# Optimization experiments

Measured on AMD Instinct MI355X. Metric: run time of the kernel, lower is better.

## Reference

```python
import jax, jax.numpy as jnp
import numpy as np

# Faithful JAX port of DNCWrapper wrapping ixaxaar/pytorch-dnc DNC:
# input_dim=output_dim=512, 2 DNC layers, 2-layer LSTM controller each,
# nr_cells=16, cell_size=20, read_heads=4, clip=20, independent_linears, batch_first.
B, T, IN, H = 128, 32, 512, 512
M, Wc, R = 16, 20, 4
RW = R * Wc                        # 80 = read-vector width
NN_IN = IN + RW                    # 592 controller input (== H + RW since IN == H)
IFACE = RW + R + Wc + 1 + Wc + Wc + R + 1 + 1 + 3 * R  # 163 interface width
L = 2                              # DNC layers
CLIP = 20.0
EPS = 1e-6                         # cosine-similarity delta
DELTA = 5e-6                       # usage floor before cumprod


def setup_inputs():
    key = jax.random.key(0)
    ks = jax.random.split(key, 13)
    p = lambda k, shape: jax.random.normal(k, shape, jnp.float32) * 0.05
    return {
        "x": jax.random.normal(ks[0], (B, T, IN), jnp.float32),
        "W_ih0": p(ks[1], (L, 4 * H, NN_IN)),
        "W_hh0": p(ks[2], (L, 4 * H, H)),
        "b_ih0": p(ks[3], (L, 4 * H)),
        "b_hh0": p(ks[4], (L, 4 * H)),
        "W_ih1": p(ks[5], (L, 4 * H, H)),
        "W_hh1": p(ks[6], (L, 4 * H, H)),
        "b_ih1": p(ks[7], (L, 4 * H)),
        "b_hh1": p(ks[8], (L, 4 * H)),
        "W_iface": p(ks[9], (L, IFACE, H)),
        "b_iface": p(ks[10], (L, IFACE)),
        "W_out": p(ks[11], (IN, H + RW)),
        "b_out": p(ks[12], (IN,)),
    }


def _lstm_cell(inp, h, c, Wih, Whh, bih, bhh):
    g = inp @ Wih.T + bih + h @ Whh.T + bhh
    i, f, gg, o = jnp.split(g, 4, axis=1)  # pytorch gate order i,f,g,o
    c = jax.nn.sigmoid(f) * c + jax.nn.sigmoid(i) * jnp.tanh(gg)
    h = jax.nn.sigmoid(o) * jnp.tanh(c)
    return h, c


def _content(mem, keys, strengths):
    # cosine-similarity content addressing, softmax over memory cells
    mn = mem / (jnp.linalg.norm(mem, axis=2, keepdims=True) + EPS)
    kn = keys / (jnp.linalg.norm(keys, axis=2, keepdims=True) + EPS)
    cos = jnp.einsum('brw,bmw->brm', kn, mn)
    return jax.nn.softmax(cos * strengths[:, :, None], axis=2)


def _memory_step(xi, mst, Wi, bi):
    memory, link, prec, rw, ww, usage = mst
    iface = xi @ Wi.T + bi
    idx = [0]
    def take(n):
        v = iface[:, idx[0]:idx[0] + n]; idx[0] += n; return v
    read_keys = jnp.tanh(take(RW)).reshape(-1, R, Wc)
    read_str = jax.nn.softplus(take(R))
    write_key = jnp.tanh(take(Wc))
    write_str = jax.nn.softplus(take(1))
    erase = jax.nn.sigmoid(take(Wc))
    write_vec = jnp.tanh(take(Wc))
    free_g = jax.nn.sigmoid(take(R))
    alloc_g = jax.nn.sigmoid(take(1))
    write_g = jax.nn.sigmoid(take(1))
    read_modes = jax.nn.softmax(take(3 * R).reshape(-1, R, 3), axis=2)
    # usage update (single write head: 1 - prod(1-ww) == ww)
    usage = usage + (1.0 - usage) * ww
    psi = jnp.prod(1.0 - free_g[:, :, None] * rw, axis=1)
    usage = usage * psi
    # content lookup with write key on pre-write memory
    wcw = _content(memory, write_key[:, None, :], write_str)[:, 0]  # (b,M)
    # allocation: ascending usage sort + exclusive cumprod, then unsort
    u = DELTA + (1.0 - DELTA) * usage
    phi = jnp.argsort(u, axis=1)
    su = jnp.take_along_axis(u, phi, axis=1)
    ones = jnp.ones((u.shape[0], 1), u.dtype)
    prod_ex = jnp.cumprod(jnp.concatenate([ones, su], axis=1), axis=1)[:, :-1]
    sa = (1.0 - su) * prod_ex
    alloc = jnp.take_along_axis(sa, jnp.argsort(phi, axis=1), axis=1)
    # write weighting
    ww = write_g * (alloc_g * alloc + (1.0 - alloc_g) * wcw)
    # erase + write
    memory = memory * (1.0 - ww[:, :, None] * erase[:, None, :]) \
             + ww[:, :, None] * write_vec[:, None, :]
    # temporal link matrix + precedence
    prev_scale = 1.0 - ww[:, :, None] - ww[:, None, :]
    link = (prev_scale * link + ww[:, :, None] * prec[:, None, :]) \
           * (1.0 - jnp.eye(M, dtype=link.dtype))
    prec = (1.0 - jnp.sum(ww, axis=1, keepdims=True)) * prec + ww
    # read: content + forward/backward link traversal, mixed by read modes
    rcw = _content(memory, read_keys, read_str)  # (b,R,M)
    fwd = jnp.einsum('bij,brj->bri', link, rw)
    bwd = jnp.einsum('bri,bij->brj', rw, link)
    rw = read_modes[:, :, 0:1] * bwd + read_modes[:, :, 1:2] * fwd + read_modes[:, :, 2:3] * rcw
    read_vecs = jnp.einsum('brm,bmw->brw', rw, memory).reshape(-1, RW)
    return read_vecs, (memory, link, prec, rw, ww, usage)


def _forward(x, W_ih0, W_hh0, b_ih0, b_hh0, W_ih1, W_hh1, b_ih1, b_hh1,
             W_iface, b_iface, W_out, b_out):
    b = x.shape[0]
    z = lambda *s: jnp.zeros(s, x.dtype)
    carry0 = (z(L, 2, b, H), z(L, 2, b, H), z(L, b, M, Wc), z(L, b, M, M),
              z(L, b, M), z(L, b, R, M), z(L, b, M), z(L, b, M))
    # repo precomputes inputs[t] = cat(x_t, initial last_read) for ALL t (last_read is
    # NOT threaded across time, only memory/LSTM state is) -- reproduced faithfully
    last_read = z(b, RW)

    def step(carry, x_t):
        h, c, mem, link, prec, rw, ww, usage = carry
        inp = jnp.concatenate([x_t, last_read], axis=1)
        new = [[] for _ in range(8)]
        for l in range(L):
            h0, c0 = _lstm_cell(inp, h[l, 0], c[l, 0], W_ih0[l], W_hh0[l], b_ih0[l], b_hh0[l])
            h1, c1 = _lstm_cell(h0, h[l, 1], c[l, 1], W_ih1[l], W_hh1[l], b_ih1[l], b_hh1[l])
            out = jnp.clip(h1, -CLIP, CLIP)
            read_vecs, mst = _memory_step(out, (mem[l], link[l], prec[l], rw[l], ww[l], usage[l]),
                                          W_iface[l], b_iface[l])
            inp = jnp.concatenate([out, read_vecs], axis=1)  # feeds next DNC layer
            new[0].append(jnp.stack([h0, h1])); new[1].append(jnp.stack([c0, c1]))
            for i, a in enumerate(mst):
                new[2 + i].append(a)
        y_t = inp @ W_out.T + b_out  # final output layer: nn_output_size -> input_size
        return tuple(jnp.stack(n) for n in new), y_t

    _, ys = jax.lax.scan(step, carry0, jnp.moveaxis(x, 1, 0))
    return jnp.moveaxis(ys, 0, 1)  # (B, T, IN), batch_first


def reference(x, W_ih0, W_hh0, b_ih0, b_hh0, W_ih1, W_hh1, b_ih1, b_hh1,
              W_iface, b_iface, W_out, b_out):
    return _forward(x, W_ih0, W_hh0, b_ih0, b_hh0, W_ih1, W_hh1, b_ih1, b_hh1,
                    W_iface, b_iface, W_out, b_out)
```

## Files before the change

kernel.cpp:

```cpp
#include <hip/hip_runtime.h>
#include <hip/hip_bf16.h>
#include <math.h>

#define B_ 128
#define T_ 32
#define IN_ 512
#define H_ 512
#define M_ 16
#define WC_ 20
#define R_ 4
#define RW_ 80
#define NNIN_ 592
#define IFACE_ 163
#define IFP_ 176
#define K1P_ 1120
#define K2P_ 1024
#define KOP_ 608
#define CLIP_ 20.0f
#define EPS_ 1e-6f
#define DELTA_ 5e-6f

typedef __bf16 bf16x8 __attribute__((ext_vector_type(8)));
typedef float f32x4 __attribute__((ext_vector_type(4)));

__device__ __forceinline__ float sigmoidf_(float x) { return 1.0f / (1.0f + __expf(-x)); }
__device__ __forceinline__ float tanhf_(float x) {
    float e = __expf(-2.f * fabsf(x));
    float t = (1.f - e) / (1.f + e);
    return copysignf(t, x);
}
__device__ __forceinline__ float softplusf_(float x) {
    return fmaxf(x, 0.0f) + log1pf(__expf(-fabsf(x)));
}
__device__ __forceinline__ void split2(float v, __bf16* hp, __bf16* lp) {
    __bf16 h = (__bf16)v;
    *hp = h;
    *lp = (__bf16)(v - (float)h);
}
#define WBAR_() __builtin_amdgcn_wave_barrier()

struct P {
    const float *x, *bih0, *bhh0, *bih1, *bhh1, *bif0, *bif1, *bout;
    float* out;
    __bf16 *a10[4];
    __bf16 *a11[4];
    __bf16 *a20[4];
    __bf16 *a21[4];
    __bf16 *y[4];
    float *c00, *c01, *c10, *c11;
    float *mem0, *link0, *prec0, *rw0, *ww0, *us0;
    float *mem1, *link1, *prec1, *rw1, *ww1, *us1;
    __bf16 *w10, *w20, *w11, *w21, *wo;
    __bf16 *wif0h, *wif0l, *wif1h, *wif1l;
    float *S0[2], *S1[2];
};

__device__ __forceinline__ void gemm_lstm_tile2(
    int tid, int jt, int mt0, float* red,
    const __bf16* A, int KS,
    const __bf16* W, int nsteps,
    const float* b1, const float* b2, float* cst,
    __bf16* d1, int st1, int off1,
    __bf16* d2, int st2, int off2, int clip2)
{
    const int wave = tid >> 6, lane = tid & 63;
    const int l15 = lane & 15, quad = lane >> 4;
    const int j0 = jt * 16, m0 = mt0 * 16;

    f32x4 acc0[4], acc1[4];
    #pragma unroll
    for (int g = 0; g < 4; ++g)
        #pragma unroll
        for (int i = 0; i < 4; ++i) { acc0[g][i] = 0.f; acc1[g][i] = 0.f; }

    const int ks = (wave * nsteps) >> 2;
    const int ke = ((wave + 1) * nsteps) >> 2;

    size_t aoff0 = (size_t)(m0 + l15) * KS + ks * 32 + quad * 8;
    size_t aoff1 = aoff0 + (size_t)16 * KS;
    size_t woff[4];
    #pragma unroll
    for (int g = 0; g < 4; ++g)
        woff[g] = (size_t)(g * 512 + j0 + l15) * KS + ks * 32 + quad * 8;

    for (int s = ks; s < ke; ++s) {
        bf16x8 ah0 = *(const bf16x8*)(A + aoff0);
        bf16x8 ah1 = *(const bf16x8*)(A + aoff1);
        aoff0 += 32; aoff1 += 32;
        #pragma unroll
        for (int g = 0; g < 4; ++g) {
            bf16x8 wh = *(const bf16x8*)(W + woff[g]);
            woff[g] += 32;
            acc0[g] = __builtin_amdgcn_mfma_f32_16x16x32_bf16(ah0, wh, acc0[g], 0, 0, 0);
            acc1[g] = __builtin_amdgcn_mfma_f32_16x16x32_bf16(ah1, wh, acc1[g], 0, 0, 0);
        }
    }

    const int col = j0 + l15;
    float bg[4];
    #pragma unroll
    for (int g = 0; g < 4; ++g) bg[g] = b1[g * 512 + col] + b2[g * 512 + col];

    #pragma unroll
    for (int pair = 0; pair < 2; ++pair) {
        #pragma unroll
        for (int g = 0; g < 4; ++g)
            #pragma unroll
            for (int r = 0; r < 4; ++r)
                red[(g * 4 + r) * 256 + wave * 64 + lane] =
                    pair ? acc1[g][r] : acc0[g][r];
        __syncthreads();

        const int m = m0 + pair * 16 + quad * 4 + wave;
        float gv[4];
        #pragma unroll
        for (int g = 0; g < 4; ++g) {
            const float* rg = red + (g * 4 + wave) * 256;
            gv[g] = rg[lane] + rg[64 + lane] + rg[128 + lane] + rg[192 + lane] + bg[g];
        }
        float cold = cst[m * H_ + col];
        float cn = sigmoidf_(gv[1]) * cold + sigmoidf_(gv[0]) * tanhf_(gv[2]);
        cst[m * H_ + col] = cn;
        float h = sigmoidf_(gv[3]) * tanhf_(cn);
        d1[(size_t)m * st1 + off1 + col] = (__bf16)h;
        float h2 = clip2 ? fminf(fmaxf(h, -CLIP_), CLIP_) : h;
        d2[(size_t)m * st2 + off2 + col] = (__bf16)h2;
        if (pair == 0) __syncthreads();
    }
}

__device__ __forceinline__ void gemm_plain_tile(
    int tid, int nt, int mt, float* red,
    const __bf16* A, int AS,
    const __bf16* W, int WS,
    int nsteps, const float* bias, float* C, int ldc)
{
    const int wave = tid >> 6, lane = tid & 63;
    const int l15 = lane & 15, quad = lane >> 4;
    const int n0 = nt * 16, m0 = mt * 16;

    f32x4 acc;
    #pragma unroll
    for (int i = 0; i < 4; ++i) acc[i] = 0.f;

    const int ks = (wave * nsteps) >> 2;
    const int ke = ((wave + 1) * nsteps) >> 2;

    size_t aoff = (size_t)(m0 + l15) * AS + ks * 32 + quad * 8;
    size_t woff = (size_t)(n0 + l15) * WS + ks * 32 + quad * 8;

    for (int s = ks; s < ke; ++s) {
        bf16x8 ah = *(const bf16x8*)(A + aoff);
        bf16x8 wh = *(const bf16x8*)(W + woff);
        aoff += 32; woff += 32;
        acc = __builtin_amdgcn_mfma_f32_16x16x32_bf16(ah, wh, acc, 0, 0, 0);
    }

    #pragma unroll
    for (int r = 0; r < 4; ++r) red[r * 256 + wave * 64 + lane] = acc[r];
    __syncthreads();

    const int col = n0 + l15;
    const int m = m0 + quad * 4 + wave;
    const float* rg = red + wave * 256;
    float v = rg[lane] + rg[64 + lane] + rg[128 + lane] + rg[192 + lane] + bias[col];
    C[(size_t)m * ldc + col] = v;
}

__device__ __forceinline__ void gemm_iface_tile(
    int tid, int jt, int mt, float* red,
    const __bf16* A, int AS,
    const __bf16* Wh, const __bf16* Wl,
    const float* bif, float* Sout)
{
    const int wave = tid >> 6, lane = tid & 63;
    const int l15 = lane & 15, quad = lane >> 4;
    const int n0 = jt * 16, m0 = mt * 16;

    f32x4 acc;
    #pragma unroll
    for (int i = 0; i < 4; ++i) acc[i] = 0.f;

    size_t aoff = (size_t)(m0 + l15) * AS + wave * 128 + quad * 8;
    size_t woff = (size_t)(n0 + l15) * 512 + wave * 128 + quad * 8;

    #pragma unroll
    for (int s = 0; s < 4; ++s) {
        bf16x8 ah = *(const bf16x8*)(A + aoff);
        bf16x8 wh = *(const bf16x8*)(Wh + woff);
        bf16x8 wl = *(const bf16x8*)(Wl + woff);
        aoff += 32; woff += 32;
        acc = __builtin_amdgcn_mfma_f32_16x16x32_bf16(ah, wh, acc, 0, 0, 0);
        acc = __builtin_amdgcn_mfma_f32_16x16x32_bf16(ah, wl, acc, 0, 0, 0);
    }

    #pragma unroll
    for (int r = 0; r < 4; ++r) red[r * 256 + wave * 64 + lane] = acc[r];
    __syncthreads();

    const int o = n0 + l15;
    if (o < IFACE_) {
        const int m = m0 + quad * 4 + wave;
        const float* rg = red + wave * 256;
        float v = rg[lane] + rg[64 + lane] + rg[128 + lane] + rg[192 + lane] + bif[o];
        float rr;
        if (o < 80)        rr = tanhf_(v);
        else if (o < 84)   rr = softplusf_(v);
        else if (o < 104)  rr = tanhf_(v);
        else if (o < 105)  rr = softplusf_(v);
        else if (o < 125)  rr = sigmoidf_(v);
        else if (o < 145)  rr = tanhf_(v);
        else if (o < 151)  rr = sigmoidf_(v);
        else               rr = v;
        Sout[(size_t)m * IFP_ + o] = rr;
    }
}

__device__ void mem_batch(int b, int wl, float* W, const float* Sbuf,
    float* mem, float* link, float* prec, float* rw,
    float* ww, float* usage, __bf16* rv, int rvst)
{
    for (int i = wl; i < IFACE_; i += 64) W[i] = Sbuf[(size_t)b * IFP_ + i];
    if (wl < M_) W[224 + wl] = prec[(size_t)b * M_ + wl];
    W[240 + wl] = rw[(size_t)b * R_ * M_ + wl];
    #pragma unroll
    for (int k = 0; k < 4; ++k)
        W[368 + wl + 64 * k] = link[(size_t)b * M_ * M_ + wl + 64 * k];
    #pragma unroll
    for (int k = 0; k < 5; ++k)
        W[624 + wl + 64 * k] = mem[(size_t)b * M_ * WC_ + wl + 64 * k];
    WBAR_();

    if (wl < R_) {
        float a0 = W[151 + wl * 3], a1 = W[152 + wl * 3], a2 = W[153 + wl * 3];
        float mx = fmaxf(a0, fmaxf(a1, a2));
        float e0 = __expf(a0 - mx), e1 = __expf(a1 - mx), e2 = __expf(a2 - mx);
        float s = e0 + e1 + e2;
        W[164 + wl * 3] = e0 / s; W[165 + wl * 3] = e1 / s; W[166 + wl * 3] = e2 / s;
    }
    WBAR_();

    if (wl < M_) {
        const int m = wl;
        float wwold = ww[(size_t)b * M_ + m];
        float u = usage[(size_t)b * M_ + m];
        u = u + (1.f - u) * wwold;
        float psi = 1.f;
        #pragma unroll
        for (int r = 0; r < R_; ++r) psi *= (1.f - W[145 + r] * W[240 + r * 16 + m]);
        u *= psi;

        float kn2 = 0.f, mn2 = 0.f, dot = 0.f;
        #pragma unroll
        for (int w = 0; w < WC_; ++w) {
            float kv = W[84 + w], mv = W[624 + m * WC_ + w];
            kn2 += kv * kv; mn2 += mv * mv; dot += kv * mv;
        }
        float c = dot / ((sqrtf(kn2) + EPS_) * (sqrtf(mn2) + EPS_)) * W[104];
        float mx = c;
        #pragma unroll
        for (int off = 8; off; off >>= 1) mx = fmaxf(mx, __shfl_xor(mx, off, 16));
        float e = __expf(c - mx);
        float se = e;
        #pragma unroll
        for (int off = 8; off; off >>= 1) se += __shfl_xor(se, off, 16);
        float wcw = e / se;

        float uu = DELTA_ + (1.f - DELTA_) * u;
        int rank = 0;
        #pragma unroll
        for (int j = 0; j < 16; ++j) {
            float uj = __shfl(uu, j, 16);
            if (uj < uu || (uj == uu && j < m)) ++rank;
        }
        float prod = 1.f;
        #pragma unroll
        for (int j = 0; j < 16; ++j) {
            float uj = __shfl(uu, j, 16);
            int   rj = __shfl(rank, j, 16);
            if (rj < rank) prod *= uj;
        }
        float alloc = (1.f - uu) * prod;

        float ag = W[149], wg = W[150];
        float wwn = wg * (ag * alloc + (1.f - ag) * wcw);
        float sw = wwn;
        #pragma unroll
        for (int off = 8; off; off >>= 1) sw += __shfl_xor(sw, off, 16);

        W[208 + m] = wwn;
        usage[(size_t)b * M_ + m] = u;
        ww[(size_t)b * M_ + m]    = wwn;
        prec[(size_t)b * M_ + m]  = (1.f - sw) * W[224 + m] + wwn;
    }
    WBAR_();

    #pragma unroll
    for (int k = 0; k < 5; ++k) {
        int i = wl + 64 * k;
        int m = i / WC_, w = i - m * WC_;
        float nm = W[624 + i] * (1.f - W[208 + m] * W[105 + w]) + W[208 + m] * W[125 + w];
        W[624 + i] = nm;
        mem[(size_t)b * M_ * WC_ + i] = nm;
    }
    #pragma unroll
    for (int k = 0; k < 4; ++k) {
        int i = wl + 64 * k;
        int ii = i >> 4, jj = i & 15;
        float v = (1.f - W[208 + ii] - W[208 + jj]) * W[368 + i] + W[208 + ii] * W[224 + jj];
        if (ii == jj) v = 0.f;
        W[368 + i] = v;
        link[(size_t)b * M_ * M_ + i] = v;
    }
    WBAR_();

    {
        const int r = wl >> 4, m = wl & 15;
        float kn2 = 0.f, mn2 = 0.f, dot = 0.f;
        #pragma unroll
        for (int w = 0; w < WC_; ++w) {
            float kv = W[r * WC_ + w], mv = W[624 + m * WC_ + w];
            kn2 += kv * kv; mn2 += mv * mv; dot += kv * mv;
        }
        float c = dot / ((sqrtf(kn2) + EPS_) * (sqrtf(mn2) + EPS_)) * W[80 + r];
        float mx = c;
        #pragma unroll
        for (int off = 8; off; off >>= 1) mx = fmaxf(mx, __shfl_xor(mx, off, 16));
        float e = __expf(c - mx);
        float se = e;
        #pragma unroll
        for (int off = 8; off; off >>= 1) se += __shfl_xor(se, off, 16);
        float rc = e / se;

        float fwd = 0.f, bwd = 0.f;
        #pragma unroll
        for (int j = 0; j < M_; ++j) fwd += W[368 + m * 16 + j] * W[240 + r * 16 + j];
        #pragma unroll
        for (int i2 = 0; i2 < M_; ++i2) bwd += W[240 + r * 16 + i2] * W[368 + i2 * 16 + m];
        float v = W[164 + r * 3 + 0] * bwd + W[164 + r * 3 + 1] * fwd + W[164 + r * 3 + 2] * rc;
        W[304 + wl] = v;
        rw[(size_t)b * R_ * M_ + wl] = v;
    }
    WBAR_();

    #pragma unroll
    for (int k = 0; k < 2; ++k) {
        int i = wl + 64 * k;
        if (i < RW_) {
            int r = i / WC_, w = i - r * WC_;
            float s = 0.f;
            #pragma unroll
            for (int m = 0; m < M_; ++m) s += W[304 + r * 16 + m] * W[624 + m * WC_ + w];
            rv[(size_t)b * rvst + IN_ + i] = (__bf16)s;
        }
    }
}

__device__ void mem_group4(int bbase, int tid, float* smem, const float* Sbuf,
    float* mem, float* link, float* prec, float* rw, float* ww, float* usage,
    __bf16* rv, int rvst)
{
    const int wave = tid >> 6, wl = tid & 63;
    mem_batch(bbase + wave, wl, smem + wave * 1024, Sbuf,
              mem, link, prec, rw, ww, usage, rv, rvst);
}

__global__ __launch_bounds__(256, 6) void slot_kernel(P p, int s)
{
    __shared__ float smem[4096];
    const int blk = blockIdx.x, tid = threadIdx.x;
    const int xcd = blk & 7, k = blk >> 3;

    if (k < 4) {
        int t = s - 3;
        if (t >= 0 && t < T_) {
            int i = xcd * 4 + k;
            mem_group4(i * 4, tid, smem, p.S0[t & 1],
                p.mem0, p.link0, p.prec0, p.rw0, p.ww0, p.us0,
                p.a11[t & 3], K1P_);
        }
    } else if (k < 8) {
        int t = s - 7;
        if (t >= 0 && t < T_) {
            int i = xcd * 4 + (k - 4);
            mem_group4(i * 4, tid, smem, p.S1[t & 1],
                p.mem1, p.link1, p.prec1, p.rw1, p.ww1, p.us1,
                p.y[t & 3], KOP_);
        }
    } else if (k < 24) {
        int t = s;
        if (t < T_) {
            int j = k - 8;
            gemm_lstm_tile2(tid, xcd * 4 + (j & 3), (j >> 2) * 2, smem,
                p.a10[t & 3], K2P_, p.w10, K2P_ / 32,
                p.bih0, p.bhh0, p.c00,
                p.a10[(t + 1) & 3], K2P_, 512,
                p.a20[t & 3], K2P_, 0, 0);
        }
    } else if (k < 40) {
        int t = s - 1;
        if (t >= 0 && t < T_) {
            int j = k - 24;
            gemm_lstm_tile2(tid, xcd * 4 + (j & 3), (j >> 2) * 2, smem,
                p.a20[t & 3], K2P_, p.w20, K2P_ / 32,
                p.bih1, p.bhh1, p.c01,
                p.a20[(t + 1) & 3], K2P_, H_,
                p.a11[t & 3], K1P_, 0, 1);
        }
    } else if (k < 56) {
        int t = s - 4;
        if (t >= 0 && t < T_) {
            int j = k - 40;
            gemm_lstm_tile2(tid, xcd * 4 + (j & 3), (j >> 2) * 2, smem,
                p.a11[t & 3], K1P_, p.w11, K1P_ / 32,
                p.bih0 + 2048, p.bhh0 + 2048, p.c10,
                p.a11[(t + 1) & 3], K1P_, NNIN_,
                p.a21[t & 3], K2P_, 0, 0);
        }
    } else if (k < 72) {
        int t = s - 5;
        if (t >= 0 && t < T_) {
            int j = k - 56;
            gemm_lstm_tile2(tid, xcd * 4 + (j & 3), (j >> 2) * 2, smem,
                p.a21[t & 3], K2P_, p.w21, K2P_ / 32,
                p.bih1 + 2048, p.bhh1 + 2048, p.c11,
                p.a21[(t + 1) & 3], K2P_, H_,
                p.y[t & 3], KOP_, 0, 1);
        }
    } else if (k < 104) {
        int t = s - 8;
        if (t >= 0 && t < T_) {
            int j = k - 72;
            gemm_plain_tile(tid, xcd * 4 + (j & 3), j >> 2, smem,
                p.y[t & 3], KOP_, p.wo, KOP_, KOP_ / 32,
                p.bout, p.out + (size_t)t * IN_, T_ * IN_);
        }
    } else if (k < 115) {
        int t = s - 2;
        if (t >= 0 && t < T_) {
            int j = k - 104;
            gemm_iface_tile(tid, j, xcd, smem,
                p.a11[t & 3], K1P_,
                p.wif0h, p.wif0l, p.bif0, p.S0[t & 1]);
        }
    } else if (k < 126) {
        int t = s - 6;
        if (t >= 0 && t < T_) {
            int j = k - 115;
            gemm_iface_tile(tid, j, xcd, smem,
                p.y[t & 3], KOP_,
                p.wif1h, p.wif1l, p.bif1, p.S1[t & 1]);
        }
    } else {
        int tn = s + 1;
        if (tn < T_) {
            int c = xcd * 4 + (k - 126);
            for (int i = c * 256 + tid; i < B_ * IN_; i += 32 * 256) {
                int b = i >> 9, j = i & 511;
                float v = p.x[((size_t)b * T_ + tn) * IN_ + j];
                p.a10[tn & 3][(size_t)b * K2P_ + j] = (__bf16)v;
            }
        }
    }
}

struct ConvArgs { const float* s1; const float* s2; __bf16* dst; int s1s, K1, K2, Kd; };
struct ConvArgs4 { ConvArgs a[4]; };

__global__ __launch_bounds__(256) void conv_lstm(ConvArgs4 ca)
{
    ConvArgs c = ca.a[blockIdx.z];
    int k = blockIdx.x * 256 + threadIdx.x;
    if (k >= c.Kd) return;
    int n = blockIdx.y;
    float v = 0.f;
    if (k < c.K1) v = c.s1[(size_t)n * c.s1s + k];
    else if (k < c.K1 + c.K2) v = c.s2[(size_t)n * c.K2 + (k - c.K1)];
    c.dst[(size_t)n * c.Kd + k] = (__bf16)v;
}

__global__ __launch_bounds__(256) void conv_hi(
    const float* __restrict__ s1, int K1, const float* __restrict__ s2, int K2,
    int Nsrc, __bf16* __restrict__ hi, int Kd)
{
    int k = blockIdx.x * 256 + threadIdx.x;
    int n = blockIdx.y;
    if (k >= Kd) return;
    float v = 0.f;
    if (n < Nsrc) {
        if (k < K1) v = s1[(size_t)n * K1 + k];
        else if (k < K1 + K2) v = s2[(size_t)n * K2 + (k - K1)];
    }
    hi[(size_t)n * Kd + k] = (__bf16)v;
}

__global__ __launch_bounds__(256) void conv_hl(
    const float* __restrict__ src, int Nsrc, int K,
    __bf16* __restrict__ hi, __bf16* __restrict__ lo)
{
    int k = blockIdx.x * 256 + threadIdx.x;
    int n = blockIdx.y;
    if (k >= K) return;
    float v = (n < Nsrc) ? src[(size_t)n * K + k] : 0.f;
    split2(v, &hi[(size_t)n * K + k], &lo[(size_t)n * K + k]);
}

__global__ __launch_bounds__(256) void build_inp(const float* __restrict__ x,
                                                 __bf16* __restrict__ a1)
{
    int idx = blockIdx.x * 256 + threadIdx.x;
    if (idx >= B_ * IN_) return;
    int b = idx >> 9, j = idx & 511;
    float v = x[(size_t)b * T_ * IN_ + j];
    a1[(size_t)b * K2P_ + j] = (__bf16)v;
}

extern "C" void kernel_launch(void* const* d_in, const int* in_sizes, int n_in,
                              void* d_out, int out_size, void* d_ws, size_t ws_size,
                              hipStream_t stream)
{
    const float* x       = (const float*)d_in[0];
    const float* W_ih0   = (const float*)d_in[1];
    const float* W_hh0   = (const float*)d_in[2];
    const float* b_ih0   = (const float*)d_in[3];
    const float* b_hh0   = (const float*)d_in[4];
    const float* W_ih1   = (const float*)d_in[5];
    const float* W_hh1   = (const float*)d_in[6];
    const float* b_ih1   = (const float*)d_in[7];
    const float* b_hh1   = (const float*)d_in[8];
    const float* W_iface = (const float*)d_in[9];
    const float* b_iface = (const float*)d_in[10];
    const float* W_out   = (const float*)d_in[11];
    const float* b_out   = (const float*)d_in[12];

    P p;
    p.x = x;
    p.bih0 = b_ih0; p.bhh0 = b_hh0; p.bih1 = b_ih1; p.bhh1 = b_hh1;
    p.bif0 = b_iface; p.bif1 = b_iface + IFACE_;
    p.bout = b_out;
    p.out = (float*)d_out;

    char* ptr = (char*)d_ws;
    auto alloc = [&](size_t bytes) { char* r = ptr; ptr += (bytes + 255) & ~(size_t)255; return r; };

    char* zstart = ptr;
    for (int q = 0; q < 4; ++q) p.a10[q] = (__bf16*)alloc(B_ * K2P_ * 2);
    for (int q = 0; q < 4; ++q) p.a11[q] = (__bf16*)alloc(B_ * K1P_ * 2);
    for (int q = 0; q < 4; ++q) p.a20[q] = (__bf16*)alloc(B_ * K2P_ * 2);
    for (int q = 0; q < 4; ++q) p.a21[q] = (__bf16*)alloc(B_ * K2P_ * 2);
    for (int q = 0; q < 4; ++q) p.y[q]   = (__bf16*)alloc(B_ * KOP_ * 2);
    p.c00 = (float*)alloc((size_t)B_ * H_ * 4);
    p.c01 = (float*)alloc((size_t)B_ * H_ * 4);
    p.c10 = (float*)alloc((size_t)B_ * H_ * 4);
    p.c11 = (float*)alloc((size_t)B_ * H_ * 4);
    p.mem0  = (float*)alloc((size_t)B_ * M_ * WC_ * 4);
    p.link0 = (float*)alloc((size_t)B_ * M_ * M_ * 4);
    p.prec0 = (float*)alloc((size_t)B_ * M_ * 4);
    p.rw0   = (float*)alloc((size_t)B_ * R_ * M_ * 4);
    p.ww0   = (float*)alloc((size_t)B_ * M_ * 4);
    p.us0   = (float*)alloc((size_t)B_ * M_ * 4);
    p.mem1  = (float*)alloc((size_t)B_ * M_ * WC_ * 4);
    p.link1 = (float*)alloc((size_t)B_ * M_ * M_ * 4);
    p.prec1 = (float*)alloc((size_t)B_ * M_ * 4);
    p.rw1   = (float*)alloc((size_t)B_ * R_ * M_ * 4);
    p.ww1   = (float*)alloc((size_t)B_ * M_ * 4);
    p.us1   = (float*)alloc((size_t)B_ * M_ * 4);
    size_t zbytes = (size_t)(ptr - zstart);

    p.w10 = (__bf16*)alloc(2048ull * K2P_ * 2);
    p.w11 = (__bf16*)alloc(2048ull * K1P_ * 2);
    p.w20 = (__bf16*)alloc(2048ull * K2P_ * 2);
    p.w21 = (__bf16*)alloc(2048ull * K2P_ * 2);
    p.wo  = (__bf16*)alloc(512ull * KOP_ * 2);
    p.wif0h = (__bf16*)alloc((size_t)IFP_ * 512 * 2);
    p.wif0l = (__bf16*)alloc((size_t)IFP_ * 512 * 2);
    p.wif1h = (__bf16*)alloc((size_t)IFP_ * 512 * 2);
    p.wif1l = (__bf16*)alloc((size_t)IFP_ * 512 * 2);
    for (int q = 0; q < 2; ++q) p.S0[q] = (float*)alloc((size_t)B_ * IFP_ * 4);
    for (int q = 0; q < 2; ++q) p.S1[q] = (float*)alloc((size_t)B_ * IFP_ * 4);

    hipMemsetAsync(zstart, 0, zbytes, stream);

    ConvArgs4 ca;
    ca.a[0] = { W_ih0,                 W_hh0,              p.w10, NNIN_, 512,   H_, K2P_ };
    ca.a[1] = { W_ih0 + 2048ull*NNIN_, W_hh0 + 2048ull*H_, p.w11, NNIN_, NNIN_, H_, K1P_ };
    ca.a[2] = { W_ih1,                 W_hh1,              p.w20, H_,    H_,    H_, K2P_ };
    ca.a[3] = { W_ih1 + 2048ull*H_,    W_hh1 + 2048ull*H_, p.w21, H_,    H_,    H_, K2P_ };
    conv_lstm<<<dim3((K1P_ + 255) / 256, 2048, 4), 256, 0, stream>>>(ca);

    conv_hi<<<dim3((KOP_ + 255) / 256, 512), 256, 0, stream>>>(
        W_out, NNIN_, nullptr, 0, 512, p.wo, KOP_);
    conv_hl<<<dim3(2, IFP_), 256, 0, stream>>>(
        W_iface, IFACE_, 512, p.wif0h, p.wif0l);
    conv_hl<<<dim3(2, IFP_), 256, 0, stream>>>(
        W_iface + (size_t)IFACE_ * 512, IFACE_, 512, p.wif1h, p.wif1l);
    build_inp<<<(B_ * IN_ + 255) / 256, 256, 0, stream>>>(x, p.a10[0]);

    for (int s = 0; s < T_ + 8; ++s) {
        slot_kernel<<<1040, 256, 0, stream>>>(p, s);
    }
}
```

Baseline: 693.7 us.

## Precompute layer-0 input projection for all timesteps and split LSTM tiles finer

Layer 0's x·W_ih contribution is hoisted out of the recurrent loop into one batched GEMM over all timesteps (gx0), so the per-step layer-0 LSTM only multiplies the 512-wide hidden state. The per-slot x-copy work is removed. LSTM tiles now cover 16 rows instead of 32, which doubles the block count per slot (1040 to 1520) and shortens each block's critical path. The cost is a large fp32 gx buffer that must be reread every step, plus weight loads that are no longer shared across two row tiles.

```diff
diff --git a/kernel.cpp b/kernel.cpp
--- a/kernel.cpp
+++ b/kernel.cpp
@@ -53,80 +53,71 @@
     __bf16 *w10, *w20, *w11, *w21, *wo;
     __bf16 *wif0h, *wif0l, *wif1h, *wif1l;
     float *S0[2], *S1[2];
+    float *gx0;
 };
 
-__device__ __forceinline__ void gemm_lstm_tile2(
-    int tid, int jt, int mt0, float* red,
-    const __bf16* A, int KS,
-    const __bf16* W, int nsteps,
-    const float* b1, const float* b2, float* cst,
+__device__ __forceinline__ void gemm_lstm_tile1(
+    int tid, int jt, int mt, float* red,
+    const __bf16* A, int AS,
+    const __bf16* W, int WS, int nsteps,
+    const float* b1, const float* b2, const float* gx, float* cst,
     __bf16* d1, int st1, int off1,
     __bf16* d2, int st2, int off2, int clip2)
 {
     const int wave = tid >> 6, lane = tid & 63;
     const int l15 = lane & 15, quad = lane >> 4;
-    const int j0 = jt * 16, m0 = mt0 * 16;
-
-    f32x4 acc0[4], acc1[4];
+    const int j0 = jt * 16, m0 = mt * 16;
+
+    f32x4 acc[4];
     #pragma unroll
     for (int g = 0; g < 4; ++g)
         #pragma unroll
-        for (int i = 0; i < 4; ++i) { acc0[g][i] = 0.f; acc1[g][i] = 0.f; }
+        for (int i = 0; i < 4; ++i) acc[g][i] = 0.f;
 
     const int ks = (wave * nsteps) >> 2;
     const int ke = ((wave + 1) * nsteps) >> 2;
 
-    size_t aoff0 = (size_t)(m0 + l15) * KS + ks * 32 + quad * 8;
-    size_t aoff1 = aoff0 + (size_t)16 * KS;
+    size_t aoff = (size_t)(m0 + l15) * AS + ks * 32 + quad * 8;
     size_t woff[4];
     #pragma unroll
     for (int g = 0; g < 4; ++g)
-        woff[g] = (size_t)(g * 512 + j0 + l15) * KS + ks * 32 + quad * 8;
+        woff[g] = (size_t)(g * 512 + j0 + l15) * WS + ks * 32 + quad * 8;
 
     for (int s = ks; s < ke; ++s) {
-        bf16x8 ah0 = *(const bf16x8*)(A + aoff0);
-        bf16x8 ah1 = *(const bf16x8*)(A + aoff1);
-        aoff0 += 32; aoff1 += 32;
+        bf16x8 ah = *(const bf16x8*)(A + aoff);
+        aoff += 32;
         #pragma unroll
         for (int g = 0; g < 4; ++g) {
             bf16x8 wh = *(const bf16x8*)(W + woff[g]);
             woff[g] += 32;
-            acc0[g] = __builtin_amdgcn_mfma_f32_16x16x32_bf16(ah0, wh, acc0[g], 0, 0, 0);
-            acc1[g] = __builtin_amdgcn_mfma_f32_16x16x32_bf16(ah1, wh, acc1[g], 0, 0, 0);
-        }
-    }
+            acc[g] = __builtin_amdgcn_mfma_f32_16x16x32_bf16(ah, wh, acc[g], 0, 0, 0);
+        }
+    }
+
+    #pragma unroll
+    for (int g = 0; g < 4; ++g)
+        #pragma unroll
+        for (int r = 0; r < 4; ++r)
+            red[(g * 4 + r) * 256 + wave * 64 + lane] = acc[g][r];
+    __syncthreads();
 
     const int col = j0 + l15;
-    float bg[4];
-    #pragma unroll
-    for (int g = 0; g < 4; ++g) bg[g] = b1[g * 512 + col] + b2[g * 512 + col];
-
-    #pragma unroll
-    for (int pair = 0; pair < 2; ++pair) {
-        #pragma unroll
-        for (int g = 0; g < 4; ++g)
-            #pragma unroll
-            for (int r = 0; r < 4; ++r)
-                red[(g * 4 + r) * 256 + wave * 64 + lane] =
-                    pair ? acc1[g][r] : acc0[g][r];
-        __syncthreads();
-
-        const int m = m0 + pair * 16 + quad * 4 + wave;
-        float gv[4];
-        #pragma unroll
-        for (int g = 0; g < 4; ++g) {
-            const float* rg = red + (g * 4 + wave) * 256;
-            gv[g] = rg[lane] + rg[64 + lane] + rg[128 + lane] + rg[192 + lane] + bg[g];
-        }
-        float cold = cst[m * H_ + col];
-        float cn = sigmoidf_(gv[1]) * cold + sigmoidf_(gv[0]) * tanhf_(gv[2]);
-        cst[m * H_ + col] = cn;
-        float h = sigmoidf_(gv[3]) * tanhf_(cn);
-        d1[(size_t)m * st1 + off1 + col] = (__bf16)h;
-        float h2 = clip2 ? fminf(fmaxf(h, -CLIP_), CLIP_) : h;
-        d2[(size_t)m * st2 + off2 + col] = (__bf16)h2;
-        if (pair == 0) __syncthreads();
-    }
+    const int m = m0 + quad * 4 + wave;
+    float gv[4];
+    #pragma unroll
+    for (int g = 0; g < 4; ++g) {
+        const float* rg = red + (g * 4 + wave) * 256;
+        gv[g] = rg[lane] + rg[64 + lane] + rg[128 + lane] + rg[192 + lane]
+              + b1[g * 512 + col] + b2[g * 512 + col];
+        if (gx) gv[g] += gx[(size_t)m * 2048 + g * 512 + col];
+    }
+    float cold = cst[m * H_ + col];
+    float cn = sigmoidf_(gv[1]) * cold + sigmoidf_(gv[0]) * tanhf_(gv[2]);
+    cst[m * H_ + col] = cn;
+    float h = sigmoidf_(gv[3]) * tanhf_(cn);
+    d1[(size_t)m * st1 + off1 + col] = (__bf16)h;
+    float h2 = clip2 ? fminf(fmaxf(h, -CLIP_), CLIP_) : h;
+    d2[(size_t)m * st2 + off2 + col] = (__bf16)h2;
 }
 
 __device__ __forceinline__ void gemm_plain_tile(
@@ -387,79 +378,69 @@
                 p.mem1, p.link1, p.prec1, p.rw1, p.ww1, p.us1,
                 p.y[t & 3], KOP_);
         }
-    } else if (k < 24) {
+    } else if (k < 40) {
         int t = s;
         if (t < T_) {
             int j = k - 8;
-            gemm_lstm_tile2(tid, xcd * 4 + (j & 3), (j >> 2) * 2, smem,
-                p.a10[t & 3], K2P_, p.w10, K2P_ / 32,
-                p.bih0, p.bhh0, p.c00,
-                p.a10[(t + 1) & 3], K2P_, 512,
+            gemm_lstm_tile1(tid, xcd * 4 + (j & 3), j >> 2, smem,
+                p.a10[t & 3], 512, p.w10 + 512, K2P_, 16,
+                p.bih0, p.bhh0, p.gx0 + (size_t)t * B_ * 2048, p.c00,
+                p.a10[(t + 1) & 3], 512, 0,
                 p.a20[t & 3], K2P_, 0, 0);
         }
-    } else if (k < 40) {
+    } else if (k < 72) {
         int t = s - 1;
         if (t >= 0 && t < T_) {
-            int j = k - 24;
-            gemm_lstm_tile2(tid, xcd * 4 + (j & 3), (j >> 2) * 2, smem,
-                p.a20[t & 3], K2P_, p.w20, K2P_ / 32,
-                p.bih1, p.bhh1, p.c01,
+            int j = k - 40;
+            gemm_lstm_tile1(tid, xcd * 4 + (j & 3), j >> 2, smem,
+                p.a20[t & 3], K2P_, p.w20, K2P_, 32,
+                p.bih1, p.bhh1, nullptr, p.c01,
                 p.a20[(t + 1) & 3], K2P_, H_,
                 p.a11[t & 3], K1P_, 0, 1);
         }
-    } else if (k < 56) {
+    } else if (k < 104) {
         int t = s - 4;
         if (t >= 0 && t < T_) {
-            int j = k - 40;
-            gemm_lstm_tile2(tid, xcd * 4 + (j & 3), (j >> 2) * 2, smem,
-                p.a11[t & 3], K1P_, p.w11, K1P_ / 32,
-                p.bih0 + 2048, p.bhh0 + 2048, p.c10,
+            int j = k - 72;
+            gemm_lstm_tile1(tid, xcd * 4 + (j & 3), j >> 2, smem,
+                p.a11[t & 3], K1P_, p.w11, K1P_, 35,
+                p.bih0 + 2048, p.bhh0 + 2048, nullptr, p.c10,
                 p.a11[(t + 1) & 3], K1P_, NNIN_,
                 p.a21[t & 3], K2P_, 0, 0);
         }
-    } else if (k < 72) {
+    } else if (k < 136) {
         int t = s - 5;
         if (t >= 0 && t < T_) {
-            int j = k - 56;
-            gemm_lstm_tile2(tid, xcd * 4 + (j & 3), (j >> 2) * 2, smem,
-                p.a21[t & 3], K2P_, p.w21, K2P_ / 32,
-                p.bih1 + 2048, p.bhh1 + 2048, p.c11,
+            int j = k - 104;
+            gemm_lstm_tile1(tid, xcd * 4 + (j & 3), j >> 2, smem,
+                p.a21[t & 3], K2P_, p.w21, K2P_, 32,
+                p.bih1 + 2048, p.bhh1 + 2048, nullptr, p.c11,
                 p.a21[(t + 1) & 3], K2P_, H_,
                 p.y[t & 3], KOP_, 0, 1);
         }
-    } else if (k < 104) {
+    } else if (k < 168) {
         int t = s - 8;
         if (t >= 0 && t < T_) {
-            int j = k - 72;
+            int j = k - 136;
             gemm_plain_tile(tid, xcd * 4 + (j & 3), j >> 2, smem,
                 p.y[t & 3], KOP_, p.wo, KOP_, KOP_ / 32,
                 p.bout, p.out + (size_t)t * IN_, T_ * IN_);
         }
-    } else if (k < 115) {
+    } else if (k < 179) {
         int t = s - 2;
         if (t >= 0 && t < T_) {
-            int j = k - 104;
+            int j = k - 168;
             gemm_iface_tile(tid, j, xcd, smem,
                 p.a11[t & 3], K1P_,
                 p.wif0h, p.wif0l, p.bif0, p.S0[t & 1]);
         }
-    } else if (k < 126) {
+    } else {
         int t = s - 6;
         if (t >= 0 && t < T_) {
-            int j = k - 115;
+            int j = k - 179;
             gemm_iface_tile(tid, j, xcd, smem,
                 p.y[t & 3], KOP_,
                 p.wif1h, p.wif1l, p.bif1, p.S1[t & 1]);
-        }
-    } else {
-        int tn = s + 1;
-        if (tn < T_) {
-            int c = xcd * 4 + (k - 126);
-            for (int i = c * 256 + tid; i < B_ * IN_; i += 32 * 256) {
-                int b = i >> 9, j = i & 511;
-                float v = p.x[((size_t)b * T_ + tn) * IN_ + j];
-                p.a10[tn & 3][(size_t)b * K2P_ + j] = (__bf16)v;
-            }
         }
     }
 }
@@ -505,14 +486,57 @@
     split2(v, &hi[(size_t)n * K + k], &lo[(size_t)n * K + k]);
 }
 
-__global__ __launch_bounds__(256) void build_inp(const float* __restrict__ x,
-                                                 __bf16* __restrict__ a1)
+__global__ __launch_bounds__(256) void conv_xb(const float* __restrict__ x,
+                                               __bf16* __restrict__ xb)
 {
     int idx = blockIdx.x * 256 + threadIdx.x;
-    if (idx >= B_ * IN_) return;
-    int b = idx >> 9, j = idx & 511;
-    float v = x[(size_t)b * T_ * IN_ + j];
-    a1[(size_t)b * K2P_ + j] = (__bf16)v;
+    if (idx >= B_ * T_ * IN_) return;
+    int b = idx / (T_ * IN_);
+    int r = idx - b * (T_ * IN_);
+    int t = r / IN_, j = r - t * IN_;
+    xb[((size_t)t * B_ + b) * IN_ + j] = (__bf16)x[idx];
+}
+
+__global__ __launch_bounds__(256) void gx_gemm(const __bf16* __restrict__ xb,
+                                               const __bf16* __restrict__ w,
+                                               float* __restrict__ gx)
+{
+    __shared__ float red[1024];
+    const int tid = threadIdx.x;
+    const int wave = tid >> 6, lane = tid & 63;
+    const int l15 = lane & 15, quad = lane >> 4;
+    const int n0 = blockIdx.x * 16, m0 = blockIdx.y * 32;
+
+    f32x4 acc0, acc1;
+    #pragma unroll
+    for (int i = 0; i < 4; ++i) { acc0[i] = 0.f; acc1[i] = 0.f; }
+
+    size_t aoff0 = (size_t)(m0 + l15) * IN_ + wave * 128 + quad * 8;
+    size_t aoff1 = aoff0 + (size_t)16 * IN_;
+    size_t woff  = (size_t)(n0 + l15) * K2P_ + wave * 128 + quad * 8;
+
+    #pragma unroll
+    for (int s = 0; s < 4; ++s) {
+        bf16x8 a0 = *(const bf16x8*)(xb + aoff0);
+        bf16x8 a1 = *(const bf16x8*)(xb + aoff1);
+        bf16x8 wh = *(const bf16x8*)(w + woff);
+        aoff0 += 32; aoff1 += 32; woff += 32;
+        acc0 = __builtin_amdgcn_mfma_f32_16x16x32_bf16(a0, wh, acc0, 0, 0, 0);
+        acc1 = __builtin_amdgcn_mfma_f32_16x16x32_bf16(a1, wh, acc1, 0, 0, 0);
+    }
+
+    #pragma unroll
+    for (int pair = 0; pair < 2; ++pair) {
+        #pragma unroll
+        for (int r = 0; r < 4; ++r)
+            red[r * 256 + wave * 64 + lane] = pair ? acc1[r] : acc0[r];
+        __syncthreads();
+        const int m = m0 + pair * 16 + quad * 4 + wave;
+        const float* rg = red + wave * 256;
+        float v = rg[lane] + rg[64 + lane] + rg[128 + lane] + rg[192 + lane];
+        gx[(size_t)m * 2048 + n0 + l15] = v;
+        if (pair == 0) __syncthreads();
+    }
 }
 
 extern "C" void kernel_launch(void* const* d_in, const int* in_sizes, int n_in,
@@ -544,7 +568,7 @@
     auto alloc = [&](size_t bytes) { char* r = ptr; ptr += (bytes + 255) & ~(size_t)255; return r; };
 
     char* zstart = ptr;
-    for (int q = 0; q < 4; ++q) p.a10[q] = (__bf16*)alloc(B_ * K2P_ * 2);
+    for (int q = 0; q < 4; ++q) p.a10[q] = (__bf16*)alloc(B_ * 512 * 2);
     for (int q = 0; q < 4; ++q) p.a11[q] = (__bf16*)alloc(B_ * K1P_ * 2);
     for (int q = 0; q < 4; ++q) p.a20[q] = (__bf16*)alloc(B_ * K2P_ * 2);
     for (int q = 0; q < 4; ++q) p.a21[q] = (__bf16*)alloc(B_ * K2P_ * 2);
@@ -578,6 +602,8 @@
     p.wif1l = (__bf16*)alloc((size_t)IFP_ * 512 * 2);
     for (int q = 0; q < 2; ++q) p.S0[q] = (float*)alloc((size_t)B_ * IFP_ * 4);
     for (int q = 0; q < 2; ++q) p.S1[q] = (float*)alloc((size_t)B_ * IFP_ * 4);
+    __bf16* xb = (__bf16*)alloc((size_t)T_ * B_ * IN_ * 2);
+    p.gx0 = (float*)alloc((size_t)T_ * B_ * 2048 * 4);
 
     hipMemsetAsync(zstart, 0, zbytes, stream);
 
@@ -594,9 +620,10 @@
         W_iface, IFACE_, 512, p.wif0h, p.wif0l);
     conv_hl<<<dim3(2, IFP_), 256, 0, stream>>>(
         W_iface + (size_t)IFACE_ * 512, IFACE_, 512, p.wif1h, p.wif1l);
-    build_inp<<<(B_ * IN_ + 255) / 256, 256, 0, stream>>>(x, p.a10[0]);
+    conv_xb<<<(B_ * T_ * IN_ + 255) / 256, 256, 0, stream>>>(x, xb);
+    gx_gemm<<<dim3(128, 128), 256, 0, stream>>>(xb, p.w10, p.gx0);
 
     for (int s = 0; s < T_ + 8; ++s) {
-        slot_kernel<<<1040, 256, 0, stream>>>(p, s);
-    }
-}
+        slot_kernel<<<1520, 256, 0, stream>>>(p, s);
+    }
+}
```

New measurement: 883.0 us. 1.27x slower.
